# Kernel optimization log

Measured on AMD Instinct MI355X. Metric: run time of the kernel, lower is better.

Reference implementation:

```python
import jax, jax.numpy as jnp
import numpy as np
from jax import lax

DIM = 1024
HID = 1536  # int(1024 * 1.5)
K = 4
C_CONST = 8.0

def setup_inputs() -> dict:
    key = jax.random.key(0)
    ks = jax.random.split(key, 9)
    x = jax.random.normal(ks[0], (4, 4096, DIM), dtype=jnp.float32)
    proj_w = jax.random.normal(ks[1], (2 * HID, DIM), dtype=jnp.float32) * DIM ** -0.5
    conv_w = jax.random.normal(ks[2], (HID, 1, K), dtype=jnp.float32) * (1.0 / K) ** 0.5
    conv_b = jnp.zeros((HID,), dtype=jnp.float32)
    ip_w = jax.random.normal(ks[3], (HID, HID), dtype=jnp.float32) * HID ** -0.5
    ip_b = jnp.zeros((HID,), dtype=jnp.float32)
    gp_w = jax.random.normal(ks[4], (HID, HID), dtype=jnp.float32) * HID ** -0.5
    gp_b = jnp.zeros((HID,), dtype=jnp.float32)
    forget_lambda = jnp.linspace(-4.323, -9.0, HID, dtype=jnp.float32)
    out_w = jax.random.normal(ks[5], (DIM, HID), dtype=jnp.float32) * HID ** -0.5
    return {"x": x, "proj_w": proj_w, "conv_w": conv_w, "conv_b": conv_b,
            "ip_w": ip_w, "ip_b": ip_b, "gp_w": gp_w, "gp_b": gp_b,
            "forget_lambda": forget_lambda, "out_w": out_w}

def _hawk(x, proj_w, conv_w, conv_b, ip_w, ip_b, gp_w, gp_b, forget_lambda, out_w):
    B, T, _ = x.shape
    # input projection -> gate, x  (each [B,T,HID])
    gx = jnp.einsum('btd,hd->bth', x, proj_w)
    gate, xh = gx[..., :HID], gx[..., HID:]
    # causal depthwise conv1d: left-pad K-1 (torch pads both sides then trims [:T])
    xc = lax.conv_general_dilated(
        xh.transpose(0, 2, 1),  # [B,HID,T]
        conv_w,                  # [HID,1,K]
        window_strides=(1,), padding=[(K - 1, 0)],
        dimension_numbers=('NCH', 'OIH', 'NCH'),
        feature_group_count=HID)
    xc = xc.transpose(0, 2, 1) + conv_b  # [B,T,HID]
    # RG-LRU gates
    rec = jax.nn.sigmoid(jnp.einsum('bth,gh->btg', xc, gp_w) + gp_b)
    inp = jax.nn.sigmoid(jnp.einsum('bth,gh->btg', xc, ip_w) + ip_b)
    alpha = jnp.exp(-C_CONST * jax.nn.softplus(forget_lambda) * rec)
    beta = jnp.sqrt(1.0 - alpha ** 2 + 1e-6)
    xbeta = beta * inp * xc
    # linear recurrence h_t = alpha_t * h_{t-1} + xbeta_t via parallel scan over time
    def combine(c1, c2):
        a1, b1 = c1
        a2, b2 = c2
        return a1 * a2, a2 * b1 + b2
    _, h = lax.associative_scan(combine, (alpha, xbeta), axis=1)
    # output: gelu(gate) * h -> dim (torch F.gelu default is exact erf form)
    return jnp.einsum('bth,dh->btd', jax.nn.gelu(gate, approximate=False) * h, out_w)

def reference(x, proj_w, conv_w, conv_b, ip_w, ip_b, gp_w, gp_b, forget_lambda, out_w):
    return _hawk(x, proj_w, conv_w, conv_b, ip_w, ip_b, gp_w, gp_b, forget_lambda, out_w)
```

## Files before the change

kernel.cpp:

```cpp
#include <hip/hip_runtime.h>
#include <cstdint>
#include <cstddef>

#define DIMX 1024
#define HID  1536
#define BB   4
#define TT   4096
#define MM   (BB*TT)
#define NPROJ (2*HID)
#define NC   256
#define CH   16
#define HB8  (HID/8)

typedef _Float16 f16x8 __attribute__((ext_vector_type(8)));
typedef float    f32x4 __attribute__((ext_vector_type(4)));

#define GLOAD_LDS16(g, l) \
  __builtin_amdgcn_global_load_lds((__attribute__((address_space(1))) const void*)(g), \
                                   (__attribute__((address_space(3))) void*)(l), 16, 0, 0)

__device__ __forceinline__ float fast_sigmoid(float z) {
  return 1.f / (1.f + __expf(-z));
}
__device__ __forceinline__ float fast_erf(float x) {
  float ax = fabsf(x);
  float t = 1.f / (1.f + 0.3275911f * ax);
  float p = t * (0.254829592f + t * (-0.284496736f + t * (1.421413741f +
            t * (-1.453152027f + t * 1.061405429f))));
  float r = 1.f - p * __expf(-ax * ax);
  return copysignf(r, x);
}

__global__ void k_cvt_all(const float* __restrict__ x,  const float* __restrict__ pw,
                          const float* __restrict__ gw, const float* __restrict__ iw,
                          const float* __restrict__ ow,
                          _Float16* __restrict__ xb, _Float16* __restrict__ pwb,
                          _Float16* __restrict__ gwb, _Float16* __restrict__ owb) {
  long i = (long)blockIdx.x * blockDim.x + threadIdx.x;
  const float* src; _Float16* dst; long o;
  if      (i < 4194304) { src = x;  dst = xb;  o = i; }
  else if (i < 4980736) { src = pw; dst = pwb; o = i - 4194304; }
  else if (i < 5570560) { src = gw; dst = gwb; o = i - 4980736; }
  else if (i < 6160384) { src = iw; dst = gwb + 2359296; o = i - 5570560; }
  else if (i < 6553600) { src = ow; dst = owb; o = i - 6160384; }
  else return;
  float4 v = ((const float4*)src)[o];
  union { _Float16 h[4]; uint64_t u; } r;
  r.h[0] = (_Float16)v.x; r.h[1] = (_Float16)v.y;
  r.h[2] = (_Float16)v.z; r.h[3] = (_Float16)v.w;
  ((uint64_t*)dst)[o] = r.u;
}

#define BM 128
#define BN 128
#define BK 64
#define GRP 8

template<int MODE>
__global__ __launch_bounds__(256) void k_gemm(
    const _Float16* __restrict__ A, const _Float16* __restrict__ B,
    float* __restrict__ Cf, _Float16* __restrict__ Ch, _Float16* __restrict__ Ch2,
    const float* __restrict__ bias, const float* __restrict__ bias2,
    const float* __restrict__ fl,
    int M, int N, int K, int gridN)
{
  __shared__ __align__(16) _Float16 sA[2][BM * BK];
  __shared__ __align__(16) _Float16 sB[2][BN * BK];
  const int tid  = threadIdx.x;
  const int wave = tid >> 6;
  const int lane = tid & 63;
  const int wr = wave >> 1, wc = wave & 1;

  const int nwg = gridDim.x;
  const int bid = blockIdx.x;
  const int xcd = bid & 7;
  const int loc = bid >> 3;
  const int rpx = (nwg >> 3) / gridN;
  const int sg  = loc / (GRP * gridN);
  const int rem = loc % (GRP * gridN);
  const int mg  = rem % GRP;
  const int nn  = rem / GRP;
  const long rowA = (long)(xcd * rpx + sg * GRP + mg) * BM;
  const long rowB = (long)nn * BN;

  const int r8  = lane >> 3;
  const int gsw = ((lane & 7) ^ r8) * 8;

  const int frow = lane & 15;
  const int pg0  = ((lane >> 4) ^ (frow & 7)) << 4;
  const int pg1  = pg0 ^ 64;

  auto stage = [&](int buf, int kt) {
    #pragma unroll
    for (int j = 0; j < 4; ++j) {
      const int ck = wave * 4 + j;
      const _Float16* ga = A + (rowA + ck * 8 + r8) * (long)K + kt + gsw;
      const _Float16* gb = B + (rowB + ck * 8 + r8) * (long)K + kt + gsw;
      GLOAD_LDS16(ga, &sA[buf][ck * 512]);
      GLOAD_LDS16(gb, &sB[buf][ck * 512]);
    }
  };

  f32x4 acc[4][4] = {};
  const int nt = K / BK;

  stage(0, 0);
  stage(1, BK);
  asm volatile("s_waitcnt vmcnt(8)" ::: "memory");
  __builtin_amdgcn_s_barrier();
  __builtin_amdgcn_sched_barrier(0);

  for (int t = 0; t < nt; ++t) {
    const int cur = t & 1;
    const char* sa = (const char*)sA[cur];
    const char* sb = (const char*)sB[cur];

    f16x8 af[4][2], bf[4][2];
    #pragma unroll
    for (int m = 0; m < 4; ++m) {
      const int rb = (wr * 64 + m * 16 + frow) * 128;
      af[m][0] = *(const f16x8*)(sa + rb + pg0);
      af[m][1] = *(const f16x8*)(sa + rb + pg1);
    }
    #pragma unroll
    for (int n = 0; n < 4; ++n) {
      const int rb = (wc * 64 + n * 16 + frow) * 128;
      bf[n][0] = *(const f16x8*)(sb + rb + pg0);
      bf[n][1] = *(const f16x8*)(sb + rb + pg1);
    }
    asm volatile("s_waitcnt lgkmcnt(0)" ::: "memory");
    __builtin_amdgcn_sched_barrier(0);
    __builtin_amdgcn_s_barrier();
    __builtin_amdgcn_sched_barrier(0);

    const bool nl = (t + 2 < nt);
    if (nl) stage(cur, (t + 2) * BK);

    __builtin_amdgcn_s_setprio(1);
    #pragma unroll
    for (int kk = 0; kk < 2; ++kk)
      #pragma unroll
      for (int m = 0; m < 4; ++m)
        #pragma unroll
        for (int n = 0; n < 4; ++n)
          acc[m][n] = __builtin_amdgcn_mfma_f32_16x16x32_f16(af[m][kk], bf[n][kk], acc[m][n], 0, 0, 0);
    __builtin_amdgcn_s_setprio(0);

    if (t + 1 < nt) {
      if (nl) { asm volatile("s_waitcnt vmcnt(8)" ::: "memory"); }
      else    { asm volatile("s_waitcnt vmcnt(0)" ::: "memory"); }
      __builtin_amdgcn_s_barrier();
      __builtin_amdgcn_sched_barrier(0);
    }
  }

  const int crow0 = (lane >> 4) * 4;
  const int ccol  = lane & 15;

  float bn[4], spn[4];
  if (MODE == 5) {
    #pragma unroll
    for (int n = 0; n < 4; ++n) {
      long c = rowB + wc * 64 + n * 16 + ccol;
      if (c < HID) {
        bn[n]  = bias[c];
        spn[n] = 8.f * log1pf(__expf(fl[c]));
      } else {
        bn[n]  = bias2[c - HID];
        spn[n] = 0.f;
      }
    }
  }

  #pragma unroll
  for (int m = 0; m < 4; ++m)
    #pragma unroll
    for (int n = 0; n < 4; ++n) {
      long r0 = rowA + wr * 64 + m * 16 + crow0;
      long c  = rowB + wc * 64 + n * 16 + ccol;
      #pragma unroll
      for (int r = 0; r < 4; ++r) {
        float v = acc[m][n][r];
        long rr = r0 + r;
        if (MODE == 1) {
          if (c < HID) {
            float ge = 0.5f * v * (1.f + fast_erf(v * 0.70710678118654752f));
            Ch[rr * (long)HID + c] = (_Float16)ge;
          } else {
            Ch2[rr * (long)HID + (c - HID)] = (_Float16)v;
          }
        } else if (MODE == 5) {
          float sig = fast_sigmoid(v + bn[n]);
          if (c < HID) Ch[rr * (long)HID + c] = (_Float16)(spn[n] * sig);
          else         Ch2[rr * (long)HID + (c - HID)] = (_Float16)sig;
        } else {
          Cf[rr * (long)N + c] = v;
        }
      }
    }
}

__global__ void k_conv(const _Float16* __restrict__ xhb, const float* __restrict__ cw,
                       const float* __restrict__ cb, _Float16* __restrict__ xch) {
  long i = (long)blockIdx.x * blockDim.x + threadIdx.x;
  if (i >= (long)(MM / 4) * HB8) return;
  const int hb = (int)(i % HB8);
  const long m4 = i / HB8;
  const long m0 = m4 * 4;
  const int t0 = (int)(m0 % TT);
  const int h0 = hb * 8;

  f16x8 rows[7];
  #pragma unroll
  for (int j = 0; j < 7; ++j) {
    if (t0 + j - 3 >= 0) {
      rows[j] = *(const f16x8*)&xhb[(m0 + j - 3) * (long)HID + h0];
    } else {
      #pragma unroll
      for (int q = 0; q < 8; ++q) rows[j][q] = (_Float16)0.f;
    }
  }
  float wgt[4][8], bias[8];
  #pragma unroll
  for (int q = 0; q < 8; ++q) {
    bias[q] = cb[h0 + q];
    #pragma unroll
    for (int k = 0; k < 4; ++k) wgt[k][q] = cw[(h0 + q) * 4 + k];
  }
  #pragma unroll
  for (int tt = 0; tt < 4; ++tt) {
    f16x8 o;
    #pragma unroll
    for (int q = 0; q < 8; ++q) {
      float acc = bias[q];
      #pragma unroll
      for (int k = 0; k < 4; ++k) acc += (float)rows[tt + k][q] * wgt[k][q];
      o[q] = (_Float16)acc;
    }
    *(f16x8*)&xch[(m0 + tt) * (long)HID + h0] = o;
  }
}

__global__ void k_scan1(const _Float16* __restrict__ sbuf, const _Float16* __restrict__ ibuf,
                        const _Float16* __restrict__ xcv,
                        float* __restrict__ Ac, float* __restrict__ Bc) {
  long i = (long)blockIdx.x * blockDim.x + threadIdx.x;
  if (i >= (long)BB * NC * HB8) return;
  const int hb = (int)(i % HB8);
  const long bc = i / HB8;
  const int c = (int)(bc % NC);
  const int b = (int)(bc / NC);
  const long base = ((long)b * TT + (long)c * CH) * HID + hb * 8;
  float A[8], Bv[8];
  #pragma unroll
  for (int j = 0; j < 8; ++j) { A[j] = 1.f; Bv[j] = 0.f; }
  #pragma unroll 4
  for (int t = 0; t < CH; ++t) {
    long idx = base + (long)t * HID;
    f16x8 sv = *(const f16x8*)&sbuf[idx];
    f16x8 iv = *(const f16x8*)&ibuf[idx];
    f16x8 xv = *(const f16x8*)&xcv[idx];
    #pragma unroll
    for (int j = 0; j < 8; ++j) {
      float a = __expf(-(float)sv[j]);
      float beta = sqrtf(1.f - a * a + 1e-6f);
      float x = beta * (float)iv[j] * (float)xv[j];
      A[j] *= a;
      Bv[j] = a * Bv[j] + x;
    }
  }
  long o = ((long)b * NC + c) * HID + hb * 8;
  #pragma unroll
  for (int j = 0; j < 8; ++j) { Ac[o + j] = A[j]; Bc[o + j] = Bv[j]; }
}

__global__ void k_scan2(const float* __restrict__ Ac, const float* __restrict__ Bc,
                        float* __restrict__ carry) {
  int i = blockIdx.x * blockDim.x + threadIdx.x;
  if (i >= BB * HID) return;
  const int h = i % HID;
  const int b = i / HID;
  float cv = 0.f;
  #pragma unroll 8
  for (int c = 0; c < NC; ++c) {
    long idx = ((long)b * NC + c) * HID + h;
    carry[idx] = cv;
    cv = Ac[idx] * cv + Bc[idx];
  }
}

__global__ void k_scan3(const _Float16* __restrict__ sbuf, const _Float16* __restrict__ ibuf,
                        const _Float16* __restrict__ xcv, const float* __restrict__ carry,
                        const _Float16* __restrict__ geluG, _Float16* __restrict__ vb) {
  long i = (long)blockIdx.x * blockDim.x + threadIdx.x;
  if (i >= (long)BB * NC * HB8) return;
  const int hb = (int)(i % HB8);
  const long bc = i / HB8;
  const int c = (int)(bc % NC);
  const int b = (int)(bc / NC);
  const long base = ((long)b * TT + (long)c * CH) * HID + hb * 8;
  const long o = ((long)b * NC + c) * HID + hb * 8;
  float hv[8];
  #pragma unroll
  for (int j = 0; j < 8; ++j) hv[j] = carry[o + j];
  #pragma unroll 4
  for (int t = 0; t < CH; ++t) {
    long idx = base + (long)t * HID;
    f16x8 sv = *(const f16x8*)&sbuf[idx];
    f16x8 iv = *(const f16x8*)&ibuf[idx];
    f16x8 xv = *(const f16x8*)&xcv[idx];
    f16x8 gv = *(const f16x8*)&geluG[idx];
    f16x8 ov;
    #pragma unroll
    for (int j = 0; j < 8; ++j) {
      float a = __expf(-(float)sv[j]);
      float beta = sqrtf(1.f - a * a + 1e-6f);
      float x = beta * (float)iv[j] * (float)xv[j];
      hv[j] = a * hv[j] + x;
      ov[j] = (_Float16)((float)gv[j] * hv[j]);
    }
    *(f16x8*)&vb[idx] = ov;
  }
}

extern "C" void kernel_launch(void* const* d_in, const int* in_sizes, int n_in,
                              void* d_out, int out_size, void* d_ws, size_t ws_size,
                              hipStream_t stream) {
  const float* x      = (const float*)d_in[0];
  const float* proj_w = (const float*)d_in[1];
  const float* conv_w = (const float*)d_in[2];
  const float* conv_b = (const float*)d_in[3];
  const float* ip_w   = (const float*)d_in[4];
  const float* ip_b   = (const float*)d_in[5];
  const float* gp_w   = (const float*)d_in[6];
  const float* gp_b   = (const float*)d_in[7];
  const float* fl     = (const float*)d_in[8];
  const float* out_w  = (const float*)d_in[9];
  float* out = (float*)d_out;
  (void)in_sizes; (void)n_in; (void)out_size;

  const size_t SZ_PW   = (size_t)NPROJ * DIMX * 2;
  const size_t SZ_GW   = (size_t)NPROJ * HID * 2;
  const size_t SZ_OW   = (size_t)DIMX * HID * 2;
  const size_t SZ_MH16 = (size_t)MM * HID * 2;
  const size_t SZ_SC   = (size_t)BB * NC * HID * 4;
  const size_t NEED = SZ_PW + SZ_GW + SZ_OW + 4 * SZ_MH16 + 3 * SZ_SC;
  if (ws_size < NEED) return;

  char* ws = (char*)d_ws;
  _Float16* pwb   = (_Float16*)(ws);
  _Float16* gwb   = (_Float16*)(ws + SZ_PW);
  _Float16* owb   = (_Float16*)(ws + SZ_PW + SZ_GW);
  char* ws2 = ws + SZ_PW + SZ_GW + SZ_OW;
  _Float16* geluG = (_Float16*)(ws2);
  _Float16* xhb   = (_Float16*)(ws2 + SZ_MH16);
  _Float16* xch   = (_Float16*)(ws2 + 2 * SZ_MH16);
  _Float16* ibuf  = (_Float16*)(ws2 + 3 * SZ_MH16);
  float*    Ac    = (float*)(ws2 + 4 * SZ_MH16);
  float*    Bc    = (float*)(ws2 + 4 * SZ_MH16 + SZ_SC);
  float*    carry = (float*)(ws2 + 4 * SZ_MH16 + 2 * SZ_SC);

  _Float16* xb    = (_Float16*)d_out;
  _Float16* sbuf  = (_Float16*)d_out;

  const int THR = 256;
  auto blocks = [&](long n) { return dim3((unsigned)((n + THR - 1) / THR)); };

  k_cvt_all<<<dim3(25600), THR, 0, stream>>>(x, proj_w, gp_w, ip_w, out_w,
                                             xb, pwb, gwb, owb);

  k_gemm<1><<<dim3((MM / BM) * (NPROJ / BN)), 256, 0, stream>>>(
      xb, pwb, nullptr, geluG, xhb, nullptr, nullptr, nullptr,
      MM, NPROJ, DIMX, NPROJ / BN);

  k_conv<<<blocks((long)(MM / 4) * HB8), THR, 0, stream>>>(xhb, conv_w, conv_b, xch);

  k_gemm<5><<<dim3((MM / BM) * (NPROJ / BN)), 256, 0, stream>>>(
      xch, gwb, nullptr, sbuf, ibuf, gp_b, ip_b, fl,
      MM, NPROJ, HID, NPROJ / BN);

  k_scan1<<<blocks((long)BB * NC * HB8), THR, 0, stream>>>(sbuf, ibuf, xch, Ac, Bc);
  k_scan2<<<blocks(BB * HID), THR, 0, stream>>>(Ac, Bc, carry);
  k_scan3<<<blocks((long)BB * NC * HB8), THR, 0, stream>>>(sbuf, ibuf, xch, carry, geluG, xhb);

  k_gemm<4><<<dim3((MM / BM) * (DIMX / BN)), 256, 0, stream>>>(
      xhb, owb, out, nullptr, nullptr, nullptr, nullptr, nullptr,
      MM, DIMX, HID, DIMX / BN);
}
```

Before: 525.5 us.

## Enlarge GEMM tiles to 256x256 with 8 waves and phased LDS pipeline

The GEMM kernel moves from 128x128 tiles on 4 waves to 256x256 tiles on 8 waves (512 threads). The K loop is split into eight phases that interleave partial global-to-LDS staging with MFMA sub-blocks, and the waves interleave over the output tile. The larger tile raises arithmetic intensity and cuts global traffic per FLOP. In exchange it uses more registers (8x4 accumulators) and more LDS, which may limit occupancy, and it produces fewer workgroups, which may cause tail effects on the smaller output GEMM.

```diff
diff --git a/kernel.cpp b/kernel.cpp
--- a/kernel.cpp
+++ b/kernel.cpp
@@ -51,13 +51,49 @@
   ((uint64_t*)dst)[o] = r.u;
 }
 
-#define BM 128
-#define BN 128
+#define BM 256
+#define BN 256
 #define BK 64
-#define GRP 8
+#define GRP2 4
+
+#define MFMA16(a, b, c) __builtin_amdgcn_mfma_f32_16x16x32_f16(a, b, c, 0, 0, 0)
+
+#define PHASE(P, STAGE_STMT, WAIT_STMT)                                      \
+  {                                                                          \
+    const char* sa_ = (const char*)sA[(P) > 4 ? 1 : 0];                      \
+    const char* sb_ = (const char*)sB[(P) > 4 ? 1 : 0];                      \
+    constexpr int m0_ = (((P) - 1) & 3) * 2;                                 \
+    if constexpr ((((P) - 1) & 3) == 0) {                                    \
+      _Pragma("unroll")                                                      \
+      for (int n = 0; n < 4; ++n) {                                          \
+        bf[n][0] = *(const f16x8*)(sb_ + Bbase + n * 8192 + pg0);            \
+        bf[n][1] = *(const f16x8*)(sb_ + Bbase + n * 8192 + pg1);            \
+      }                                                                      \
+    }                                                                        \
+    f16x8 a00 = *(const f16x8*)(sa_ + Abase + (m0_    ) * 4096 + pg0);       \
+    f16x8 a01 = *(const f16x8*)(sa_ + Abase + (m0_    ) * 4096 + pg1);       \
+    f16x8 a10 = *(const f16x8*)(sa_ + Abase + (m0_ + 1) * 4096 + pg0);       \
+    f16x8 a11 = *(const f16x8*)(sa_ + Abase + (m0_ + 1) * 4096 + pg1);       \
+    STAGE_STMT;                                                              \
+    __builtin_amdgcn_s_barrier();                                            \
+    asm volatile("s_waitcnt lgkmcnt(0)" ::: "memory");                       \
+    __builtin_amdgcn_sched_barrier(0);                                       \
+    __builtin_amdgcn_s_setprio(1);                                           \
+    _Pragma("unroll")                                                        \
+    for (int n = 0; n < 4; ++n) {                                            \
+      acc[m0_][n]     = MFMA16(a00, bf[n][0], acc[m0_][n]);                  \
+      acc[m0_][n]     = MFMA16(a01, bf[n][1], acc[m0_][n]);                  \
+      acc[m0_ + 1][n] = MFMA16(a10, bf[n][0], acc[m0_ + 1][n]);              \
+      acc[m0_ + 1][n] = MFMA16(a11, bf[n][1], acc[m0_ + 1][n]);              \
+    }                                                                        \
+    __builtin_amdgcn_s_setprio(0);                                           \
+    WAIT_STMT;                                                               \
+    __builtin_amdgcn_s_barrier();                                            \
+    __builtin_amdgcn_sched_barrier(0);                                       \
+  }
 
 template<int MODE>
-__global__ __launch_bounds__(256) void k_gemm(
+__global__ __launch_bounds__(512, 2) void k_gemm(
     const _Float16* __restrict__ A, const _Float16* __restrict__ B,
     float* __restrict__ Cf, _Float16* __restrict__ Ch, _Float16* __restrict__ Ch2,
     const float* __restrict__ bias, const float* __restrict__ bias2,
@@ -69,99 +105,79 @@
   const int tid  = threadIdx.x;
   const int wave = tid >> 6;
   const int lane = tid & 63;
-  const int wr = wave >> 1, wc = wave & 1;
+  const int wr = wave >> 2, wc = wave & 3;
 
   const int nwg = gridDim.x;
   const int bid = blockIdx.x;
   const int xcd = bid & 7;
   const int loc = bid >> 3;
   const int rpx = (nwg >> 3) / gridN;
-  const int sg  = loc / (GRP * gridN);
-  const int rem = loc % (GRP * gridN);
-  const int mg  = rem % GRP;
-  const int nn  = rem / GRP;
-  const long rowA = (long)(xcd * rpx + sg * GRP + mg) * BM;
+  const int sg  = loc / (GRP2 * gridN);
+  const int rem = loc % (GRP2 * gridN);
+  const int mg  = rem % GRP2;
+  const int nn  = rem / GRP2;
+  const long rowA = (long)(xcd * rpx + sg * GRP2 + mg) * BM;
   const long rowB = (long)nn * BN;
 
   const int r8  = lane >> 3;
   const int gsw = ((lane & 7) ^ r8) * 8;
+
+  auto stA = [&](int buf, int h, int kt) {
+    const _Float16* g = A + (rowA + h * 128 + wave * 8 + r8) * (long)K + kt + gsw;
+    GLOAD_LDS16(g,                &sA[buf][(h * 128      + wave * 8) * 64]);
+    GLOAD_LDS16(g + 64 * (long)K, &sA[buf][(h * 128 + 64 + wave * 8) * 64]);
+  };
+  auto stB = [&](int buf, int h, int kt) {
+    const _Float16* g = B + (rowB + h * 128 + wave * 8 + r8) * (long)K + kt + gsw;
+    GLOAD_LDS16(g,                &sB[buf][(h * 128      + wave * 8) * 64]);
+    GLOAD_LDS16(g + 64 * (long)K, &sB[buf][(h * 128 + 64 + wave * 8) * 64]);
+  };
 
   const int frow = lane & 15;
   const int pg0  = ((lane >> 4) ^ (frow & 7)) << 4;
   const int pg1  = pg0 ^ 64;
-
-  auto stage = [&](int buf, int kt) {
-    #pragma unroll
-    for (int j = 0; j < 4; ++j) {
-      const int ck = wave * 4 + j;
-      const _Float16* ga = A + (rowA + ck * 8 + r8) * (long)K + kt + gsw;
-      const _Float16* gb = B + (rowB + ck * 8 + r8) * (long)K + kt + gsw;
-      GLOAD_LDS16(ga, &sA[buf][ck * 512]);
-      GLOAD_LDS16(gb, &sB[buf][ck * 512]);
-    }
-  };
-
-  f32x4 acc[4][4] = {};
-  const int nt = K / BK;
-
-  stage(0, 0);
-  stage(1, BK);
-  asm volatile("s_waitcnt vmcnt(8)" ::: "memory");
+  const int Abase = (wr * 16 + frow) * 128;
+  const int Bbase = (wc * 16 + frow) * 128;
+
+  const int nt    = K / BK;
+  const int nIter = nt / 2;
+
+  stB(0, 0, 0);  stB(0, 1, 0);  stA(0, 0, 0);  stA(0, 1, 0);
+  stB(1, 0, BK); stB(1, 1, BK); stA(1, 0, BK);
+  asm volatile("s_waitcnt vmcnt(6)" ::: "memory");
   __builtin_amdgcn_s_barrier();
   __builtin_amdgcn_sched_barrier(0);
 
-  for (int t = 0; t < nt; ++t) {
-    const int cur = t & 1;
-    const char* sa = (const char*)sA[cur];
-    const char* sb = (const char*)sB[cur];
-
-    f16x8 af[4][2], bf[4][2];
-    #pragma unroll
-    for (int m = 0; m < 4; ++m) {
-      const int rb = (wr * 64 + m * 16 + frow) * 128;
-      af[m][0] = *(const f16x8*)(sa + rb + pg0);
-      af[m][1] = *(const f16x8*)(sa + rb + pg1);
-    }
-    #pragma unroll
-    for (int n = 0; n < 4; ++n) {
-      const int rb = (wc * 64 + n * 16 + frow) * 128;
-      bf[n][0] = *(const f16x8*)(sb + rb + pg0);
-      bf[n][1] = *(const f16x8*)(sb + rb + pg1);
-    }
-    asm volatile("s_waitcnt lgkmcnt(0)" ::: "memory");
-    __builtin_amdgcn_sched_barrier(0);
-    __builtin_amdgcn_s_barrier();
-    __builtin_amdgcn_sched_barrier(0);
-
-    const bool nl = (t + 2 < nt);
-    if (nl) stage(cur, (t + 2) * BK);
-
-    __builtin_amdgcn_s_setprio(1);
-    #pragma unroll
-    for (int kk = 0; kk < 2; ++kk)
-      #pragma unroll
-      for (int m = 0; m < 4; ++m)
-        #pragma unroll
-        for (int n = 0; n < 4; ++n)
-          acc[m][n] = __builtin_amdgcn_mfma_f32_16x16x32_f16(af[m][kk], bf[n][kk], acc[m][n], 0, 0, 0);
-    __builtin_amdgcn_s_setprio(0);
-
-    if (t + 1 < nt) {
-      if (nl) { asm volatile("s_waitcnt vmcnt(8)" ::: "memory"); }
-      else    { asm volatile("s_waitcnt vmcnt(0)" ::: "memory"); }
-      __builtin_amdgcn_s_barrier();
-      __builtin_amdgcn_sched_barrier(0);
-    }
-  }
-
-  const int crow0 = (lane >> 4) * 4;
-  const int ccol  = lane & 15;
+  f32x4 acc[8][4] = {};
+  f16x8 bf[4][2];
+
+  for (int it = 0; it < nIter; ++it) {
+    const bool nl  = (it + 1 < nIter);
+    const int kt1 = (2 * it + 1) * BK;
+    const int ke  = (2 * it + 2) * BK;
+    const int ko  = (2 * it + 3) * BK;
+    PHASE(1, { stA(1, 1, kt1); }, {});
+    PHASE(2, { if (nl) stB(0, 0, ke); }, {});
+    PHASE(3, { if (nl) stB(0, 1, ke); }, {});
+    PHASE(4, { if (nl) stA(0, 0, ke); },
+             { if (nl) { asm volatile("s_waitcnt vmcnt(6)" ::: "memory"); }
+               else    { asm volatile("s_waitcnt vmcnt(0)" ::: "memory"); } });
+    PHASE(5, { if (nl) stA(0, 1, ke); }, {});
+    PHASE(6, { if (nl) stB(1, 0, ko); }, {});
+    PHASE(7, { if (nl) stB(1, 1, ko); }, {});
+    PHASE(8, { if (nl) stA(1, 0, ko); },
+             { if (nl) { asm volatile("s_waitcnt vmcnt(6)" ::: "memory"); }
+               else    { asm volatile("s_waitcnt vmcnt(0)" ::: "memory"); } });
+  }
+
+  const int q4   = (lane >> 4) * 4;
+  const int ccol = lane & 15;
 
   float bn[4], spn[4];
   if (MODE == 5) {
     #pragma unroll
     for (int n = 0; n < 4; ++n) {
-      long c = rowB + wc * 64 + n * 16 + ccol;
+      long c = rowB + n * 64 + wc * 16 + ccol;
       if (c < HID) {
         bn[n]  = bias[c];
         spn[n] = 8.f * log1pf(__expf(fl[c]));
@@ -173,11 +189,11 @@
   }
 
   #pragma unroll
-  for (int m = 0; m < 4; ++m)
+  for (int m = 0; m < 8; ++m)
     #pragma unroll
     for (int n = 0; n < 4; ++n) {
-      long r0 = rowA + wr * 64 + m * 16 + crow0;
-      long c  = rowB + wc * 64 + n * 16 + ccol;
+      long r0 = rowA + m * 32 + wr * 16 + q4;
+      long c  = rowB + n * 64 + wc * 16 + ccol;
       #pragma unroll
       for (int r = 0; r < 4; ++r) {
         float v = acc[m][n][r];
@@ -369,13 +385,13 @@
   k_cvt_all<<<dim3(25600), THR, 0, stream>>>(x, proj_w, gp_w, ip_w, out_w,
                                              xb, pwb, gwb, owb);
 
-  k_gemm<1><<<dim3((MM / BM) * (NPROJ / BN)), 256, 0, stream>>>(
+  k_gemm<1><<<dim3((MM / BM) * (NPROJ / BN)), 512, 0, stream>>>(
       xb, pwb, nullptr, geluG, xhb, nullptr, nullptr, nullptr,
       MM, NPROJ, DIMX, NPROJ / BN);
 
   k_conv<<<blocks((long)(MM / 4) * HB8), THR, 0, stream>>>(xhb, conv_w, conv_b, xch);
 
-  k_gemm<5><<<dim3((MM / BM) * (NPROJ / BN)), 256, 0, stream>>>(
+  k_gemm<5><<<dim3((MM / BM) * (NPROJ / BN)), 512, 0, stream>>>(
       xch, gwb, nullptr, sbuf, ibuf, gp_b, ip_b, fl,
       MM, NPROJ, HID, NPROJ / BN);
 
@@ -383,7 +399,7 @@
   k_scan2<<<blocks(BB * HID), THR, 0, stream>>>(Ac, Bc, carry);
   k_scan3<<<blocks((long)BB * NC * HB8), THR, 0, stream>>>(sbuf, ibuf, xch, carry, geluG, xhb);
 
-  k_gemm<4><<<dim3((MM / BM) * (DIMX / BN)), 256, 0, stream>>>(
+  k_gemm<4><<<dim3((MM / BM) * (DIMX / BN)), 512, 0, stream>>>(
       xhb, owb, out, nullptr, nullptr, nullptr, nullptr, nullptr,
       MM, DIMX, HID, DIMX / BN);
 }
```

New measurement: 636.6 us. +21.1%, slower.
